# Performance work log

Hardware: AMD Instinct MI355X
Metric: run time of the kernel (lower is better)

## Reference

```python
import jax, jax.numpy as jnp
import numpy as np
from jax import lax

G, N, S, K, R = 8, 4096, 2048, 64, 0.4   # graphs, nodes/graph, fps samples (ratio=0.5), max neighbors, radius
EPER = 65536                              # edges per graph (avg degree 16)
C = 13                                    # num_classes


def setup_inputs():
    key = jax.random.key(0)
    ks = jax.random.split(key, 8)
    norm = jax.random.normal(ks[0], (G * N, 3), jnp.float32)
    pos = jax.random.uniform(ks[1], (G * N, 3), jnp.float32)
    x = jax.random.normal(ks[2], (G * N, 2), jnp.float32)
    e = jax.random.randint(ks[3], (2, G, EPER), 0, N)
    off = (jnp.arange(G) * N)[None, :, None]
    edge_index = (e + off).reshape(2, G * EPER).astype(jnp.int64)
    batch = jnp.repeat(jnp.arange(G), N).astype(jnp.int64)
    def lin(k, i, o):
        return jax.random.normal(k, (i, o), jnp.float32) / np.float32(np.sqrt(i))
    W1 = lin(ks[4], 8, 64);    b1 = jnp.zeros((64,), jnp.float32)
    W2 = lin(ks[5], 72, 128);  b2 = jnp.zeros((128,), jnp.float32)
    W3 = lin(ks[6], 139, 256); b3 = jnp.zeros((256,), jnp.float32)
    lin_w = lin(ks[7], 256, C); lin_b = jnp.zeros((C,), jnp.float32)
    return dict(norm=norm, pos=pos, x=x, edge_index=edge_index, batch=batch,
                W1=W1, b1=b1, W2=W2, b2=b2, W3=W3, b3=b3, lin_w=lin_w, lin_b=lin_b)


def _gcn(h, src, dst, ew, W, b, n):
    # GCNConv(normalize=False): out[dst] += ew * (h @ W)[src]; + bias
    m = (h @ W)[src] * ew[:, None]
    return jax.ops.segment_sum(m, dst, num_segments=n) + b


def _fps(p):  # farthest point sampling on one graph, p: [N,3] -> [S] local indices (start at node 0)
    def step(carry, _):
        mind, cur = carry
        d = jnp.sum((p - p[cur]) ** 2, axis=1)
        mind = jnp.minimum(mind, d)
        return (mind, jnp.argmax(mind).astype(jnp.int32)), cur
    _, idx = lax.scan(step, (jnp.full((N,), jnp.inf, p.dtype), jnp.int32(0)), None, length=S)
    return idx


def _radius(p, q):  # p [N,3], q [S,3] -> neighbor cols [S,K] (lowest-index-first within radius), valid mask
    d2 = jnp.sum((q[:, None, :] - p[None, :, :]) ** 2, axis=-1)  # [S,N]
    mask = d2 < R * R
    score = jnp.where(mask, N - jnp.arange(N, dtype=jnp.int32)[None, :], 0)
    vals, cols = lax.top_k(score, K)
    valid = vals > 0
    return jnp.where(valid, cols, 0), valid


def reference(norm, pos, x, edge_index, batch, W1, b1, W2, b2, W3, b3, lin_w, lin_b):
    NT = G * N
    inp = jnp.concatenate([norm, pos, x], axis=1)          # [NT, 8]
    src, dst = edge_index[0], edge_index[1]
    ew = jnp.ones((src.shape[0],), inp.dtype)
    # dropout is inactive at inference (training=False)
    h1 = jax.nn.relu(_gcn(inp, src, dst, ew, W1, b1, NT))  # [NT, 64]
    h1 = jnp.concatenate([h1, inp], axis=1)                # [NT, 72]
    h2 = jax.nn.relu(_gcn(h1, src, dst, ew, W2, b2, NT))   # [NT, 128]

    pg = pos.reshape(G, N, 3)
    pgs = lax.stop_gradient(pg)
    idx_loc = jax.vmap(_fps)(pgs)                          # [G, S] local indices
    q = jax.vmap(lambda p, i: p[i])(pg, idx_loc)           # [G, S, 3] sampled positions
    cols, valid = jax.vmap(_radius)(pgs, lax.stop_gradient(q))  # [G, S, K]

    # PointConv with identity local_nn/global_nn: max over neighbors of [x_j, pos_j - pos_i]
    hg = h2.reshape(G, N, 128)
    def pconv(h, p, qv, c, v):
        msg = jnp.concatenate([h[c], p[c] - qv[:, None, :]], axis=-1)  # [S, K, 131]
        msg = jnp.where(v[..., None], msg, -jnp.inf)
        return jnp.max(msg, axis=1)                                    # [S, 131]
    x_int = jax.vmap(pconv)(hg, pg, q, cols, valid).reshape(G * S, 131)

    # filter_adj: keep edges with both endpoints sampled, remap to new ids
    idx_flat = (idx_loc + (jnp.arange(G) * N)[:, None]).reshape(-1)    # [G*S] global indices
    mapping = jnp.full((NT,), -1, jnp.int32).at[idx_flat].set(jnp.arange(G * S, dtype=jnp.int32))
    ns, nd = mapping[src], mapping[dst]
    em = (ns >= 0) & (nd >= 0)
    ew3 = em.astype(inp.dtype)
    ns = jnp.where(em, ns, 0)
    nd = jnp.where(em, nd, 0)

    h3in = jnp.concatenate([x_int, inp[idx_flat]], axis=1)  # [G*S, 139]
    h3 = jax.nn.relu(_gcn(h3in, ns, nd, ew3, W3, b3, G * S))  # [G*S, 256]

    pooled = h3.reshape(G, S, 256).max(axis=1)              # global_max_pool -> [G, 256]
    logits = pooled @ lin_w + lin_b
    out = jax.nn.log_softmax(logits, axis=1)
    pred = jax.nn.softmax(out, axis=1)
    return (out, pred)
```

## Files before the change

kernel.cpp:

```cpp
#include <hip/hip_runtime.h>
#include <hip/hip_bf16.h>

constexpr int NG   = 8;
constexpr int NPG  = 4096;
constexpr int NT   = NG * NPG;
constexpr int NS   = 2048;
constexpr int GS   = NG * NS;
constexpr int KN   = 64;
constexpr int NE   = NG * 65536;
constexpr int NC   = 13;
constexpr int NWORK = 248;

__device__ __forceinline__ float inp_val(const float* norm, const float* pos, const float* x,
                                         int node, int dim) {
  if (dim < 3) return norm[(size_t)node * 3 + dim];
  if (dim < 6) return pos[(size_t)node * 3 + (dim - 3)];
  return x[(size_t)node * 2 + (dim - 6)];
}

__device__ __forceinline__ void wbar(int* ctrs, int k, int target) {
  __syncthreads();
  __threadfence();
  if (threadIdx.x == 0) {
    __hip_atomic_fetch_add(&ctrs[k], 1, __ATOMIC_RELEASE, __HIP_MEMORY_SCOPE_AGENT);
    while (__hip_atomic_load(&ctrs[k], __ATOMIC_ACQUIRE, __HIP_MEMORY_SCOPE_AGENT) < target)
      __builtin_amdgcn_s_sleep(16);
  }
  __syncthreads();
}

__global__ __launch_bounds__(256, 1) void phaseA_kernel(
    const float* __restrict__ pos, int* __restrict__ idxf, float* __restrict__ qpos,
    const float* __restrict__ norm, const float* __restrict__ x,
    const float* __restrict__ W1, float* __restrict__ t1,
    const int* __restrict__ ei, int* __restrict__ deg,
    int* __restrict__ off1, int* __restrict__ cur1, int* __restrict__ el1,
    const float* __restrict__ b1, const float* __restrict__ W2, float* __restrict__ t2,
    const float* __restrict__ b2, float* __restrict__ h2,
    int* __restrict__ wctr) {
  if (blockIdx.x >= 8) {
    const int wb = blockIdx.x - 8;
    const int sub = threadIdx.x >> 6;
    const int f = threadIdx.x & 63;
    __shared__ float wrow[4][80];
    __shared__ int sscan[256];
    for (int n0 = wb * 4; n0 < NT; n0 += NWORK * 4) {
      int n = n0 + sub;
      if (f < 8) wrow[sub][f] = inp_val(norm, pos, x, n, f);
      float acc = 0.f;
#pragma unroll
      for (int i = 0; i < 8; ++i) acc += wrow[sub][i] * W1[i * 64 + f];
      t1[(size_t)n * 64 + f] = acc;
    }
    for (int e = wb * 256 + threadIdx.x; e < NE; e += NWORK * 256)
      atomicAdd(&deg[ei[NE + e]], 1);
    wbar(wctr, 0, NWORK);
    if (wb == 0) {
      int t = threadIdx.x, base = t * 128, s = 0;
      for (int i = 0; i < 128; ++i) s += deg[base + i];
      sscan[t] = s;
      __syncthreads();
      for (int d = 1; d < 256; d <<= 1) {
        int v = (t >= d) ? sscan[t - d] : 0;
        __syncthreads();
        sscan[t] += v;
        __syncthreads();
      }
      int excl = (t == 0) ? 0 : sscan[t - 1];
      for (int i = 0; i < 128; ++i) { off1[base + i] = excl; excl += deg[base + i]; }
      if (t == 255) off1[NT] = sscan[255];
    }
    wbar(wctr, 1, NWORK);
    for (int e = wb * 256 + threadIdx.x; e < NE; e += NWORK * 256) {
      int sN = ei[e], dN = ei[NE + e];
      int p = off1[dN] + atomicAdd(&cur1[dN], 1);
      el1[p] = sN;
    }
    wbar(wctr, 2, NWORK);
    for (int n0 = wb * 4; n0 < NT; n0 += NWORK * 4) {
      int n = n0 + sub;
      int e0 = off1[n], e1 = off1[n + 1];
      float acc = 0.f;
      for (int j = e0; j < e1; ++j) acc += t1[(size_t)el1[j] * 64 + f];
      wrow[sub][f] = fmaxf(acc + b1[f], 0.f);
      if (f < 8) wrow[sub][64 + f] = inp_val(norm, pos, x, n, f);
      float a0 = 0.f, a1 = 0.f;
#pragma unroll 8
      for (int i = 0; i < 72; ++i) {
        float r = wrow[sub][i];
        a0 += r * W2[i * 128 + f];
        a1 += r * W2[i * 128 + 64 + f];
      }
      t2[(size_t)n * 128 + f] = a0;
      t2[(size_t)n * 128 + 64 + f] = a1;
    }
    wbar(wctr, 3, NWORK);
    {
      const int f2 = threadIdx.x & 127, sub2 = threadIdx.x >> 7;
      for (int n0 = wb * 2; n0 < NT; n0 += NWORK * 2) {
        int n = n0 + sub2;
        int e0 = off1[n], e1 = off1[n + 1];
        float acc = 0.f;
        for (int j = e0; j < e1; ++j) acc += t2[(size_t)el1[j] * 128 + f2];
        h2[(size_t)n * 128 + f2] = fmaxf(acc + b2[f2], 0.f);
      }
    }
    return;
  }
  const int g = blockIdx.x;
  __shared__ float4 sq[2][4];
  __shared__ int sidx[2][4];
  __shared__ float4 qrec[NS];
  __shared__ int irec[NS];
  const float* pg = pos + (size_t)g * NPG * 3;
  const int tid = threadIdx.x;
  const int wave = tid >> 6, lane = tid & 63;
  const int p0 = tid * 16;

  float a[48];
  {
    const float4* pg4 = reinterpret_cast<const float4*>(pg + (size_t)p0 * 3);
#pragma unroll
    for (int j = 0; j < 12; ++j) {
      float4 t = pg4[j];
      a[4 * j + 0] = t.x; a[4 * j + 1] = t.y; a[4 * j + 2] = t.z; a[4 * j + 3] = t.w;
    }
  }
  float px[16], py[16], pz[16], mind[16];
#pragma unroll
  for (int i = 0; i < 16; ++i) {
    px[i] = a[3 * i]; py[i] = a[3 * i + 1]; pz[i] = a[3 * i + 2];
    mind[i] = __int_as_float(0x7f800000);
  }
  float cx = pg[0], cy = pg[1], cz = pg[2];
  int idx_sel = 0;

  for (int s = 0; s < NS; ++s) {
    if (tid == 0) { irec[s] = idx_sel; qrec[s] = make_float4(cx, cy, cz, 0.f); }
    float bestv = -1.f, bx = 0.f, by = 0.f, bz = 0.f;
    int bi = 0;
#pragma unroll
    for (int i = 0; i < 16; ++i) {
      float dx = __fsub_rn(px[i], cx);
      float dy = __fsub_rn(py[i], cy);
      float dz = __fsub_rn(pz[i], cz);
      float dd = __fadd_rn(__fadd_rn(__fmul_rn(dx, dx), __fmul_rn(dy, dy)), __fmul_rn(dz, dz));
      float nm = fminf(mind[i], dd);
      mind[i] = nm;
      bool gt = nm > bestv;
      bestv = gt ? nm : bestv;
      bx = gt ? px[i] : bx;
      by = gt ? py[i] : by;
      bz = gt ? pz[i] : bz;
      bi = gt ? i : bi;
    }
    float v = bestv;
    v = fmaxf(v, __int_as_float(__builtin_amdgcn_update_dpp(0, __float_as_int(v), 0x111, 0xF, 0xF, true)));
    v = fmaxf(v, __int_as_float(__builtin_amdgcn_update_dpp(0, __float_as_int(v), 0x112, 0xF, 0xF, true)));
    v = fmaxf(v, __int_as_float(__builtin_amdgcn_update_dpp(0, __float_as_int(v), 0x114, 0xF, 0xF, true)));
    v = fmaxf(v, __int_as_float(__builtin_amdgcn_update_dpp(0, __float_as_int(v), 0x118, 0xF, 0xF, true)));
    v = fmaxf(v, __int_as_float(__builtin_amdgcn_update_dpp(0, __float_as_int(v), 0x142, 0xF, 0xF, true)));
    v = fmaxf(v, __int_as_float(__builtin_amdgcn_update_dpp(0, __float_as_int(v), 0x143, 0xF, 0xF, true)));
    int maxbits = __builtin_amdgcn_readlane(__float_as_int(v), 63);
    float wavemax = __int_as_float(maxbits);
    unsigned long long ball = __ballot(bestv == wavemax);
    int winner = __ffsll(ball) - 1;
    int b = s & 1;
    if (lane == winner) {
      sq[b][wave] = make_float4(bx, by, bz, wavemax);
      sidx[b][wave] = p0 + bi;
    }
    __syncthreads();
    float4 q0 = sq[b][0], q1 = sq[b][1], q2 = sq[b][2], q3 = sq[b][3];
    float4 qs = q3;
    if (q2.w >= qs.w) qs = q2;
    if (q1.w >= qs.w) qs = q1;
    if (q0.w >= qs.w) qs = q0;
    cx = qs.x; cy = qs.y; cz = qs.z;
    if (tid == 0) {
      int i0 = sidx[b][0], i1 = sidx[b][1], i2 = sidx[b][2], i3 = sidx[b][3];
      float r = q3.w; int is = i3;
      if (q2.w >= r) { r = q2.w; is = i2; }
      if (q1.w >= r) { r = q1.w; is = i1; }
      if (q0.w >= r) { r = q0.w; is = i0; }
      idx_sel = is;
    }
  }
  __syncthreads();
  for (int j = tid; j < NS; j += 256) {
    idxf[g * NS + j] = g * NPG + irec[j];
    float4 q = qrec[j];
    size_t m = (size_t)(g * NS + j) * 3;
    qpos[m + 0] = q.x; qpos[m + 1] = q.y; qpos[m + 2] = q.z;
  }
}

__global__ void featdeg_kernel(const float* __restrict__ xint, const int* __restrict__ idxf,
                               const float* __restrict__ norm, const float* __restrict__ pos,
                               const float* __restrict__ x, const float* __restrict__ W3,
                               float* __restrict__ t3,
                               const int* __restrict__ ei, const int* __restrict__ mp,
                               int* __restrict__ deg) {
  if (blockIdx.x >= GS) {
    int e = (blockIdx.x - GS) * 256 + threadIdx.x;
    int ns = mp[ei[e]], nd = mp[ei[NE + e]];
    if (ns >= 0 && nd >= 0) atomicAdd(&deg[nd], 1);
    return;
  }
  int m = blockIdx.x, f = threadIdx.x;
  __shared__ float row[139];
  if (f < 131) row[f] = xint[(size_t)m * 131 + f];
  else if (f < 139) { int node = idxf[m]; row[f] = inp_val(norm, pos, x, node, f - 131); }
  __syncthreads();
  float acc = 0.f;
#pragma unroll 8
  for (int i = 0; i < 139; ++i) acc += row[i] * W3[i * 256 + f];
  t3[(size_t)m * 256 + f] = acc;
}

__global__ void fill2_kernel(const int* __restrict__ ei, const int* __restrict__ mp,
                             const int* __restrict__ off, int* __restrict__ cur,
                             int* __restrict__ el) {
  int e = blockIdx.x * 256 + threadIdx.x;
  if (e < NE) {
    int ns = mp[ei[e]], nd = mp[ei[NE + e]];
    if (ns >= 0 && nd >= 0) {
      int p = off[nd] + atomicAdd(&cur[nd], 1);
      el[p] = ns;
    }
  }
}

__global__ __launch_bounds__(1024) void scan_kernel(const int* __restrict__ in,
                                                    int* __restrict__ out, int n) {
  __shared__ int ls[1024];
  int tid = threadIdx.x;
  int per = (n + 1023) >> 10;
  int base = tid * per;
  int s = 0;
  for (int i = 0; i < per; ++i) { int idx = base + i; if (idx < n) s += in[idx]; }
  ls[tid] = s;
  __syncthreads();
  for (int d = 1; d < 1024; d <<= 1) {
    int v = (tid >= d) ? ls[tid - d] : 0;
    __syncthreads();
    ls[tid] += v;
    __syncthreads();
  }
  int excl = (tid == 0) ? 0 : ls[tid - 1];
  for (int i = 0; i < per; ++i) {
    int idx = base + i;
    if (idx < n) { out[idx] = excl; excl += in[idx]; }
  }
  if (tid == 1023) out[n] = ls[1023];
}

__global__ void agg_kernel(const float* __restrict__ t, const int* __restrict__ off,
                           const int* __restrict__ el, const float* __restrict__ b,
                           float* __restrict__ out, int F) {
  int node = blockIdx.x, f = threadIdx.x;
  int e0 = off[node], e1 = off[node + 1];
  float acc = 0.f;
  for (int j = e0; j < e1; ++j) acc += t[(size_t)el[j] * F + f];
  out[(size_t)node * F + f] = fmaxf(acc + b[f], 0.f);
}

__global__ __launch_bounds__(256) void radius_kernel(const float* __restrict__ pos,
                                                     const float* __restrict__ qpos,
                                                     int* __restrict__ cols,
                                                     int* __restrict__ cnt,
                                                     const int* __restrict__ idxf,
                                                     int* __restrict__ mp) {
  const int g = blockIdx.x;
  __shared__ float sx[NPG], sy[NPG], sz[NPG];
  const float* pg = pos + (size_t)g * NPG * 3;
  for (int i = threadIdx.x; i < NPG * 3; i += 256) {
    float v = pg[i]; int node = i / 3, c = i - node * 3;
    if (c == 0) sx[node] = v; else if (c == 1) sy[node] = v; else sz[node] = v;
  }
  __syncthreads();
  int m = g * NS + blockIdx.y * 256 + threadIdx.x;
  mp[idxf[m]] = m;
  float qx = qpos[(size_t)m * 3], qy = qpos[(size_t)m * 3 + 1], qz = qpos[(size_t)m * 3 + 2];
  int* out = cols + (size_t)m * KN;
  int c = 0;
  for (int i = 0; i < NPG; ++i) {
    float dx = __fsub_rn(sx[i], qx);
    float dy = __fsub_rn(sy[i], qy);
    float dz = __fsub_rn(sz[i], qz);
    float d2 = __fadd_rn(__fadd_rn(__fmul_rn(dx, dx), __fmul_rn(dy, dy)), __fmul_rn(dz, dz));
    if (d2 < 0.16f) {
      out[c++] = i;
      if (c == KN) break;
    }
  }
  cnt[m] = c;
}

__global__ __launch_bounds__(64) void pointconv_kernel(const float* __restrict__ h2,
                                                       const float* __restrict__ pos,
                                                       const float* __restrict__ qpos,
                                                       const int* __restrict__ cols,
                                                       const int* __restrict__ cnt,
                                                       float* __restrict__ xint) {
  int m = blockIdx.x, t = threadIdx.x;
  int g = m / NS;
  int n = cnt[m];
  const int* cl = cols + (size_t)m * KN;
  float m0 = -INFINITY, m1 = -INFINITY, mp = -INFINITY;
  for (int k = 0; k < n; ++k) {
    int c = cl[k];
    size_t base = (size_t)(g * NPG + c);
    m0 = fmaxf(m0, h2[base * 128 + t]);
    m1 = fmaxf(m1, h2[base * 128 + 64 + t]);
    if (t < 3) mp = fmaxf(mp, pos[base * 3 + t]);
  }
  float* xo = xint + (size_t)m * 131;
  xo[t] = m0;
  xo[64 + t] = m1;
  if (t < 3) xo[128 + t] = __fsub_rn(mp, qpos[(size_t)m * 3 + t]);
}

__global__ void pool_kernel(const float* __restrict__ h3, float* __restrict__ pooled) {
  int g = blockIdx.x, ch = blockIdx.y, f = threadIdx.x;
  float mx = 0.f;
  size_t base = ((size_t)g * NS + (size_t)ch * 256) * 256 + f;
  for (int s = 0; s < 256; ++s) mx = fmaxf(mx, h3[base + (size_t)s * 256]);
  atomicMax((int*)pooled + g * 256 + f, __float_as_int(mx));
}

__global__ void head_kernel(const float* __restrict__ pooled, const float* __restrict__ lw,
                            const float* __restrict__ lb, float* __restrict__ outp) {
  __shared__ float lg[NG * NC];
  int t = threadIdx.x;
  if (t < NG * NC) {
    int g = t / NC, c = t % NC;
    float acc = lb[c];
    for (int k = 0; k < 256; ++k) acc += pooled[g * 256 + k] * lw[k * NC + c];
    lg[t] = acc;
  }
  __syncthreads();
  if (t < NG) {
    int g = t;
    float mx = -INFINITY;
    for (int c = 0; c < NC; ++c) mx = fmaxf(mx, lg[g * NC + c]);
    float sum = 0.f;
    for (int c = 0; c < NC; ++c) sum += expf(lg[g * NC + c] - mx);
    float lse = logf(sum);
    float ov[NC];
    float mx2 = -INFINITY;
    for (int c = 0; c < NC; ++c) {
      ov[c] = lg[g * NC + c] - mx - lse;
      outp[g * NC + c] = ov[c];
      mx2 = fmaxf(mx2, ov[c]);
    }
    float s2 = 0.f;
    for (int c = 0; c < NC; ++c) s2 += expf(ov[c] - mx2);
    for (int c = 0; c < NC; ++c) outp[NG * NC + g * NC + c] = expf(ov[c] - mx2) / s2;
  }
}

extern "C" void kernel_launch(void* const* d_in, const int* in_sizes, int n_in,
                              void* d_out, int out_size, void* d_ws, size_t ws_size,
                              hipStream_t stream) {
  const float* norm = (const float*)d_in[0];
  const float* pos  = (const float*)d_in[1];
  const float* x    = (const float*)d_in[2];
  const int* ei     = (const int*)d_in[3];
  const float* W1 = (const float*)d_in[5];
  const float* b1 = (const float*)d_in[6];
  const float* W2 = (const float*)d_in[7];
  const float* b2 = (const float*)d_in[8];
  const float* W3 = (const float*)d_in[9];
  const float* b3 = (const float*)d_in[10];
  const float* lw = (const float*)d_in[11];
  const float* lb = (const float*)d_in[12];
  float* outp = (float*)d_out;

  char* w = (char*)d_ws;
  size_t o = 0;
  auto alloc = [&](size_t bytes) -> void* {
    void* p = w + o;
    o = (o + bytes + 255) & ~(size_t)255;
    return p;
  };
  float* A    = (float*)alloc((size_t)NT * 128 * 4);
  float* Bf   = (float*)alloc((size_t)NT * 128 * 4);
  float* T1   = (float*)alloc((size_t)NT * 64 * 4);
  float* xint = (float*)alloc((size_t)GS * 131 * 4);
  int* cols   = (int*)alloc((size_t)GS * KN * 4);
  int* cnt    = (int*)alloc((size_t)GS * 4);
  int* deg1   = (int*)alloc((size_t)NT * 4);
  int* off1   = (int*)alloc((size_t)(NT + 1) * 4);
  int* cur1   = (int*)alloc((size_t)NT * 4);
  int* el1    = (int*)alloc((size_t)NE * 4);
  int* deg2   = (int*)alloc((size_t)GS * 4);
  int* off2   = (int*)alloc((size_t)(GS + 1) * 4);
  int* cur2   = (int*)alloc((size_t)GS * 4);
  int* el2    = (int*)alloc((size_t)NE * 4);
  int* idxf   = (int*)alloc((size_t)GS * 4);
  float* qpos = (float*)alloc((size_t)GS * 3 * 4);
  int* mapv   = (int*)alloc((size_t)NT * 4);
  float* pooled = (float*)alloc((size_t)NG * 256 * 4);
  int* wctr   = (int*)alloc(64);

  hipMemsetAsync(deg1, 0, (size_t)NT * 4, stream);
  hipMemsetAsync(cur1, 0, (size_t)NT * 4, stream);
  hipMemsetAsync(deg2, 0, (size_t)GS * 4, stream);
  hipMemsetAsync(cur2, 0, (size_t)GS * 4, stream);
  hipMemsetAsync(mapv, 0xFF, (size_t)NT * 4, stream);
  hipMemsetAsync(pooled, 0, (size_t)NG * 256 * 4, stream);
  hipMemsetAsync(wctr, 0, 64, stream);

  {
    void* ka[] = {(void*)&pos, (void*)&idxf, (void*)&qpos, (void*)&norm, (void*)&x,
                  (void*)&W1, (void*)&T1, (void*)&ei, (void*)&deg1,
                  (void*)&off1, (void*)&cur1, (void*)&el1,
                  (void*)&b1, (void*)&W2, (void*)&A, (void*)&b2, (void*)&Bf,
                  (void*)&wctr};
    hipLaunchCooperativeKernel((const void*)phaseA_kernel, dim3(8 + NWORK), dim3(256),
                               ka, 0, stream);
  }
  radius_kernel<<<dim3(NG, NS / 256), 256, 0, stream>>>(pos, qpos, cols, cnt, idxf, mapv);
  pointconv_kernel<<<GS, 64, 0, stream>>>(Bf, pos, qpos, cols, cnt, xint);
  featdeg_kernel<<<GS + NE / 256, 256, 0, stream>>>(xint, idxf, norm, pos, x, W3, A,
                                                    ei, mapv, deg2);
  scan_kernel<<<1, 1024, 0, stream>>>(deg2, off2, GS);
  fill2_kernel<<<NE / 256, 256, 0, stream>>>(ei, mapv, off2, cur2, el2);
  agg_kernel<<<GS, 256, 0, stream>>>(A, off2, el2, b3, Bf, 256);
  pool_kernel<<<dim3(NG, NS / 256), 256, 0, stream>>>(Bf, pooled);
  head_kernel<<<1, 128, 0, stream>>>(pooled, lw, lb, outp);
}
```

Measured before the change: 2.166 ms.

## Split radius search across 4 threads per query, batch W3 GEMM, fuse pooling into aggregation

```diff
diff --git a/kernel.cpp b/kernel.cpp
--- a/kernel.cpp
+++ b/kernel.cpp
@@ -10,6 +10,8 @@
 constexpr int NE   = NG * 65536;
 constexpr int NC   = 13;
 constexpr int NWORK = 248;
+constexpr int SPB  = 16;
+constexpr int NF3B = GS / SPB;
 
 __device__ __forceinline__ float inp_val(const float* norm, const float* pos, const float* x,
                                          int node, int dim) {
@@ -195,106 +197,48 @@
   }
 }
 
-__global__ void featdeg_kernel(const float* __restrict__ xint, const int* __restrict__ idxf,
-                               const float* __restrict__ norm, const float* __restrict__ pos,
-                               const float* __restrict__ x, const float* __restrict__ W3,
-                               float* __restrict__ t3,
-                               const int* __restrict__ ei, const int* __restrict__ mp,
-                               int* __restrict__ deg) {
-  if (blockIdx.x >= GS) {
-    int e = (blockIdx.x - GS) * 256 + threadIdx.x;
-    int ns = mp[ei[e]], nd = mp[ei[NE + e]];
-    if (ns >= 0 && nd >= 0) atomicAdd(&deg[nd], 1);
-    return;
-  }
-  int m = blockIdx.x, f = threadIdx.x;
-  __shared__ float row[139];
-  if (f < 131) row[f] = xint[(size_t)m * 131 + f];
-  else if (f < 139) { int node = idxf[m]; row[f] = inp_val(norm, pos, x, node, f - 131); }
-  __syncthreads();
-  float acc = 0.f;
-#pragma unroll 8
-  for (int i = 0; i < 139; ++i) acc += row[i] * W3[i * 256 + f];
-  t3[(size_t)m * 256 + f] = acc;
-}
-
-__global__ void fill2_kernel(const int* __restrict__ ei, const int* __restrict__ mp,
-                             const int* __restrict__ off, int* __restrict__ cur,
-                             int* __restrict__ el) {
-  int e = blockIdx.x * 256 + threadIdx.x;
-  if (e < NE) {
-    int ns = mp[ei[e]], nd = mp[ei[NE + e]];
-    if (ns >= 0 && nd >= 0) {
-      int p = off[nd] + atomicAdd(&cur[nd], 1);
-      el[p] = ns;
-    }
-  }
-}
-
-__global__ __launch_bounds__(1024) void scan_kernel(const int* __restrict__ in,
-                                                    int* __restrict__ out, int n) {
-  __shared__ int ls[1024];
-  int tid = threadIdx.x;
-  int per = (n + 1023) >> 10;
-  int base = tid * per;
-  int s = 0;
-  for (int i = 0; i < per; ++i) { int idx = base + i; if (idx < n) s += in[idx]; }
-  ls[tid] = s;
-  __syncthreads();
-  for (int d = 1; d < 1024; d <<= 1) {
-    int v = (tid >= d) ? ls[tid - d] : 0;
-    __syncthreads();
-    ls[tid] += v;
-    __syncthreads();
-  }
-  int excl = (tid == 0) ? 0 : ls[tid - 1];
-  for (int i = 0; i < per; ++i) {
-    int idx = base + i;
-    if (idx < n) { out[idx] = excl; excl += in[idx]; }
-  }
-  if (tid == 1023) out[n] = ls[1023];
-}
-
-__global__ void agg_kernel(const float* __restrict__ t, const int* __restrict__ off,
-                           const int* __restrict__ el, const float* __restrict__ b,
-                           float* __restrict__ out, int F) {
-  int node = blockIdx.x, f = threadIdx.x;
-  int e0 = off[node], e1 = off[node + 1];
-  float acc = 0.f;
-  for (int j = e0; j < e1; ++j) acc += t[(size_t)el[j] * F + f];
-  out[(size_t)node * F + f] = fmaxf(acc + b[f], 0.f);
-}
-
-__global__ __launch_bounds__(256) void radius_kernel(const float* __restrict__ pos,
-                                                     const float* __restrict__ qpos,
-                                                     int* __restrict__ cols,
-                                                     int* __restrict__ cnt,
-                                                     const int* __restrict__ idxf,
-                                                     int* __restrict__ mp) {
-  const int g = blockIdx.x;
-  __shared__ float sx[NPG], sy[NPG], sz[NPG];
-  const float* pg = pos + (size_t)g * NPG * 3;
+__global__ __launch_bounds__(256, 1) void radius_kernel(
+    const float* __restrict__ pos, const float* __restrict__ qpos,
+    int* __restrict__ cols, int* __restrict__ cnt,
+    const int* __restrict__ idxf, int* __restrict__ mp) {
+  __shared__ float spx[NPG], spy[NPG], spz[NPG];
+  __shared__ int sbuf[KN][64][4];
+  const int g = blockIdx.x >> 5;
+  const int s0 = (blockIdx.x & 31) * 64;
+  const float* pgc = pos + (size_t)g * NPG * 3;
   for (int i = threadIdx.x; i < NPG * 3; i += 256) {
-    float v = pg[i]; int node = i / 3, c = i - node * 3;
-    if (c == 0) sx[node] = v; else if (c == 1) sy[node] = v; else sz[node] = v;
-  }
-  __syncthreads();
-  int m = g * NS + blockIdx.y * 256 + threadIdx.x;
-  mp[idxf[m]] = m;
-  float qx = qpos[(size_t)m * 3], qy = qpos[(size_t)m * 3 + 1], qz = qpos[(size_t)m * 3 + 2];
-  int* out = cols + (size_t)m * KN;
+    float v = pgc[i]; int node = i / 3, cc = i - node * 3;
+    if (cc == 0) spx[node] = v; else if (cc == 1) spy[node] = v; else spz[node] = v;
+  }
+  __syncthreads();
+  const int group = threadIdx.x >> 2;
+  const int j = threadIdx.x & 3;
+  const int m = g * NS + s0 + group;
+  if (j == 0) mp[idxf[m]] = m;
+  const float qx = qpos[(size_t)m * 3], qy = qpos[(size_t)m * 3 + 1],
+              qz = qpos[(size_t)m * 3 + 2];
   int c = 0;
-  for (int i = 0; i < NPG; ++i) {
-    float dx = __fsub_rn(sx[i], qx);
-    float dy = __fsub_rn(sy[i], qy);
-    float dz = __fsub_rn(sz[i], qz);
+  const int i0 = j * 1024;
+  for (int i = i0; i < i0 + 1024; ++i) {
+    float dx = __fsub_rn(spx[i], qx);
+    float dy = __fsub_rn(spy[i], qy);
+    float dz = __fsub_rn(spz[i], qz);
     float d2 = __fadd_rn(__fadd_rn(__fmul_rn(dx, dx), __fmul_rn(dy, dy)), __fmul_rn(dz, dz));
     if (d2 < 0.16f) {
-      out[c++] = i;
-      if (c == KN) break;
-    }
-  }
-  cnt[m] = c;
+      sbuf[c][group][j] = i;
+      if (++c == KN) break;
+    }
+  }
+  const int lbase = (threadIdx.x & 63) & ~3;
+  int c0 = __shfl(c, lbase + 0), c1 = __shfl(c, lbase + 1),
+      c2 = __shfl(c, lbase + 2), c3 = __shfl(c, lbase + 3);
+  int pre = (j > 0 ? c0 : 0) + (j > 1 ? c1 : 0) + (j > 2 ? c2 : 0);
+  int total = c0 + c1 + c2 + c3;
+  if (j == 0) cnt[m] = total < KN ? total : KN;
+  int take = KN - pre;
+  take = take < 0 ? 0 : (take > c ? c : take);
+  int* outp = cols + (size_t)m * KN + pre;
+  for (int i = 0; i < take; ++i) outp[i] = sbuf[i][group][j];
 }
 
 __global__ __launch_bounds__(64) void pointconv_kernel(const float* __restrict__ h2,
@@ -321,12 +265,87 @@
   if (t < 3) xo[128 + t] = __fsub_rn(mp, qpos[(size_t)m * 3 + t]);
 }
 
-__global__ void pool_kernel(const float* __restrict__ h3, float* __restrict__ pooled) {
-  int g = blockIdx.x, ch = blockIdx.y, f = threadIdx.x;
-  float mx = 0.f;
-  size_t base = ((size_t)g * NS + (size_t)ch * 256) * 256 + f;
-  for (int s = 0; s < 256; ++s) mx = fmaxf(mx, h3[base + (size_t)s * 256]);
-  atomicMax((int*)pooled + g * 256 + f, __float_as_int(mx));
+__global__ void post2_kernel(const float* __restrict__ xint, const int* __restrict__ idxf,
+                             const float* __restrict__ norm, const float* __restrict__ pos,
+                             const float* __restrict__ x, const float* __restrict__ W3,
+                             float* __restrict__ t3,
+                             const int* __restrict__ ei, const int* __restrict__ mp,
+                             int* __restrict__ deg) {
+  if (blockIdx.x >= NF3B) {
+    int e = (blockIdx.x - NF3B) * 256 + threadIdx.x;
+    int ns = mp[ei[e]], nd = mp[ei[NE + e]];
+    if (ns >= 0 && nd >= 0) atomicAdd(&deg[nd], 1);
+    return;
+  }
+  __shared__ float srow[SPB][140];
+  const int m0 = blockIdx.x * SPB;
+  for (int jj = threadIdx.x; jj < SPB * 139; jj += 256) {
+    int sub = jj / 139, i = jj - sub * 139;
+    int m = m0 + sub;
+    srow[sub][i] = (i < 131) ? xint[(size_t)m * 131 + i]
+                             : inp_val(norm, pos, x, idxf[m], i - 131);
+  }
+  __syncthreads();
+  int f = threadIdx.x;
+  float acc[SPB];
+#pragma unroll
+  for (int s = 0; s < SPB; ++s) acc[s] = 0.f;
+#pragma unroll 4
+  for (int i = 0; i < 139; ++i) {
+    float wv = W3[i * 256 + f];
+#pragma unroll
+    for (int s = 0; s < SPB; ++s) acc[s] += srow[s][i] * wv;
+  }
+#pragma unroll
+  for (int s = 0; s < SPB; ++s) t3[(size_t)(m0 + s) * 256 + f] = acc[s];
+}
+
+__global__ void fill2_kernel(const int* __restrict__ ei, const int* __restrict__ mp,
+                             const int* __restrict__ off, int* __restrict__ cur,
+                             int* __restrict__ el) {
+  int e = blockIdx.x * 256 + threadIdx.x;
+  if (e < NE) {
+    int ns = mp[ei[e]], nd = mp[ei[NE + e]];
+    if (ns >= 0 && nd >= 0) {
+      int p = off[nd] + atomicAdd(&cur[nd], 1);
+      el[p] = ns;
+    }
+  }
+}
+
+__global__ __launch_bounds__(1024) void scan_kernel(const int* __restrict__ in,
+                                                    int* __restrict__ out, int n) {
+  __shared__ int ls[1024];
+  int tid = threadIdx.x;
+  int per = (n + 1023) >> 10;
+  int base = tid * per;
+  int s = 0;
+  for (int i = 0; i < per; ++i) { int idx = base + i; if (idx < n) s += in[idx]; }
+  ls[tid] = s;
+  __syncthreads();
+  for (int d = 1; d < 1024; d <<= 1) {
+    int v = (tid >= d) ? ls[tid - d] : 0;
+    __syncthreads();
+    ls[tid] += v;
+    __syncthreads();
+  }
+  int excl = (tid == 0) ? 0 : ls[tid - 1];
+  for (int i = 0; i < per; ++i) {
+    int idx = base + i;
+    if (idx < n) { out[idx] = excl; excl += in[idx]; }
+  }
+  if (tid == 1023) out[n] = ls[1023];
+}
+
+__global__ void aggpool_kernel(const float* __restrict__ t, const int* __restrict__ off,
+                               const int* __restrict__ el, const float* __restrict__ b,
+                               float* __restrict__ pooled) {
+  int node = blockIdx.x, f = threadIdx.x;
+  int e0 = off[node], e1 = off[node + 1];
+  float acc = 0.f;
+  for (int j = e0; j < e1; ++j) acc += t[(size_t)el[j] * 256 + f];
+  float val = fmaxf(acc + b[f], 0.f);
+  atomicMax((int*)pooled + (node >> 11) * 256 + f, __float_as_int(val));
 }
 
 __global__ void head_kernel(const float* __restrict__ pooled, const float* __restrict__ lw,
@@ -402,7 +421,7 @@
   float* qpos = (float*)alloc((size_t)GS * 3 * 4);
   int* mapv   = (int*)alloc((size_t)NT * 4);
   float* pooled = (float*)alloc((size_t)NG * 256 * 4);
-  int* wctr   = (int*)alloc(64);
+  int* wctr   = (int*)alloc(128);
 
   hipMemsetAsync(deg1, 0, (size_t)NT * 4, stream);
   hipMemsetAsync(cur1, 0, (size_t)NT * 4, stream);
@@ -410,7 +429,7 @@
   hipMemsetAsync(cur2, 0, (size_t)GS * 4, stream);
   hipMemsetAsync(mapv, 0xFF, (size_t)NT * 4, stream);
   hipMemsetAsync(pooled, 0, (size_t)NG * 256 * 4, stream);
-  hipMemsetAsync(wctr, 0, 64, stream);
+  hipMemsetAsync(wctr, 0, 128, stream);
 
   {
     void* ka[] = {(void*)&pos, (void*)&idxf, (void*)&qpos, (void*)&norm, (void*)&x,
@@ -421,13 +440,12 @@
     hipLaunchCooperativeKernel((const void*)phaseA_kernel, dim3(8 + NWORK), dim3(256),
                                ka, 0, stream);
   }
-  radius_kernel<<<dim3(NG, NS / 256), 256, 0, stream>>>(pos, qpos, cols, cnt, idxf, mapv);
+  radius_kernel<<<256, 256, 0, stream>>>(pos, qpos, cols, cnt, idxf, mapv);
   pointconv_kernel<<<GS, 64, 0, stream>>>(Bf, pos, qpos, cols, cnt, xint);
-  featdeg_kernel<<<GS + NE / 256, 256, 0, stream>>>(xint, idxf, norm, pos, x, W3, A,
+  post2_kernel<<<NF3B + NE / 256, 256, 0, stream>>>(xint, idxf, norm, pos, x, W3, A,
                                                     ei, mapv, deg2);
   scan_kernel<<<1, 1024, 0, stream>>>(deg2, off2, GS);
   fill2_kernel<<<NE / 256, 256, 0, stream>>>(ei, mapv, off2, cur2, el2);
-  agg_kernel<<<GS, 256, 0, stream>>>(A, off2, el2, b3, Bf, 256);
-  pool_kernel<<<dim3(NG, NS / 256), 256, 0, stream>>>(Bf, pooled);
+  aggpool_kernel<<<GS, 256, 0, stream>>>(A, off2, el2, b3, pooled);
   head_kernel<<<1, 128, 0, stream>>>(pooled, lw, lb, outp);
 }
```

New measurement: 2.069 ms. -4.5%, faster.
